# Kernel optimization log

Measured on AMD Instinct MI355X. Metric: run time of the kernel, lower is better.

Reference implementation:

```python
import jax, jax.numpy as jnp
import numpy as np

N_IN, N_H = 512, 1024

def setup_inputs() -> dict:
    key = jax.random.key(0)
    ks = jax.random.split(key, 20)
    s_in = 1.0 / np.sqrt(N_IN)
    s_h = 1.0 / np.sqrt(N_H)
    inp = {
        'x': jax.random.normal(ks[0], (64, 256, N_IN), jnp.float32),
        'c': jax.random.normal(ks[1], (64, 256, N_H), jnp.float32),
        'h': jax.random.normal(ks[2], (64, 256, N_H), jnp.float32),
    }
    names_in = ['ii', 'if_', 'ig', 'io']
    names_h = ['hi', 'hf', 'hg', 'ho']
    k = 3
    for n in names_in:
        inp['W_' + n] = jax.random.uniform(ks[k], (N_H, N_IN), jnp.float32, -s_in, s_in); k += 1
        inp['b_' + n] = jax.random.uniform(ks[k], (N_H,), jnp.float32, -s_in, s_in); k += 1
    for n in names_h:
        inp['W_' + n] = jax.random.uniform(ks[k], (N_H, N_H), jnp.float32, -s_h, s_h); k += 1
        inp['b_' + n] = jax.random.uniform(ks[k], (N_H,), jnp.float32, -s_h, s_h); k += 1
    return inp

def reference(x, c, h,
              W_ii, b_ii, W_if_, b_if_, W_ig, b_ig, W_io, b_io,
              W_hi, b_hi, W_hf, b_hf, W_hg, b_hg, W_ho, b_ho):
    # Fuse the 4 input-side and 4 hidden-side linears into two GEMMs.
    Wx = jnp.concatenate([W_ii, W_if_, W_ig, W_io], axis=0)   # [4H, n_in]
    Wh = jnp.concatenate([W_hi, W_hf, W_hg, W_ho], axis=0)   # [4H, n_h]
    bx = jnp.concatenate([b_ii, b_if_, b_ig, b_io], axis=0)
    bh = jnp.concatenate([b_hi, b_hf, b_hg, b_ho], axis=0)
    z = jnp.einsum('sad,gd->sag', x, Wx) + jnp.einsum('sad,gd->sag', h, Wh) + bx + bh  # [S,A,4H]
    zi, zf, zg, zo = jnp.split(z, 4, axis=-1)
    i_t = jax.nn.sigmoid(zi)
    f_t = jax.nn.sigmoid(zf)
    g_t = jnp.tanh(zg)
    o_t = jax.nn.sigmoid(zo)
    c_t = f_t * c + i_t * g_t
    h_t = o_t * jnp.tanh(c_t)
    return (c_t, h_t)
```

## Files before the change

kernel.cpp:

```cpp
#include <hip/hip_runtime.h>
#include <hip/hip_bf16.h>

#define M_ROWS 16384
#define N_IN   512
#define N_HID  1024
#define K_TOT  1536
#define N_TOT  4096
#define NT     48

typedef __attribute__((ext_vector_type(4))) float f32x4;
typedef __attribute__((ext_vector_type(8))) short bf16x8;
typedef __attribute__((ext_vector_type(4))) int   i32x4;

__device__ __forceinline__ ushort f2bf(float f) {
    union { float f; unsigned u; } un; un.f = f;
    unsigned u = un.u;
    u += 0x7fffu + ((u >> 16) & 1u);
    return (ushort)(u >> 16);
}

__device__ __forceinline__ bf16x8 as_bf(i32x4 v) {
    union { i32x4 i; bf16x8 b; } u; u.i = v; return u.b;
}


__global__ void build_A(const float* __restrict__ x, const float* __restrict__ h,
                        ushort* __restrict__ A) {
    const int total = M_ROWS * K_TOT / 4;
    for (int p = blockIdx.x * blockDim.x + threadIdx.x; p < total;
         p += gridDim.x * blockDim.x) {
        int flat = p * 4;
        int row = flat / K_TOT;
        int col = flat - row * K_TOT;
        const float* src = (col < N_IN)
            ? (x + (size_t)row * N_IN + col)
            : (h + (size_t)row * N_HID + (col - N_IN));
        float4 v = *(const float4*)src;
        ushort4 o;
        o.x = f2bf(v.x); o.y = f2bf(v.y); o.z = f2bf(v.z); o.w = f2bf(v.w);
        *(ushort4*)(A + flat) = o;
    }
}

__global__ void build_W(const float* __restrict__ Wii, const float* __restrict__ Wif,
                        const float* __restrict__ Wig, const float* __restrict__ Wio,
                        const float* __restrict__ Whi, const float* __restrict__ Whf,
                        const float* __restrict__ Whg, const float* __restrict__ Who,
                        ushort* __restrict__ Wp) {
    const int total = N_TOT * K_TOT / 4;
    for (int p = blockIdx.x * blockDim.x + threadIdx.x; p < total;
         p += gridDim.x * blockDim.x) {
        int flat = p * 4;
        int prow = flat / K_TOT;
        int col = flat - prow * K_TOT;
        int bn  = prow >> 8;
        int r   = prow & 255;
        int wcn = r >> 6;
        int g   = (r >> 4) & 3;
        int u   = r & 15;
        int j   = bn * 64 + wcn * 16 + u;
        const float* src;
        if (col < N_IN) {
            const float* Wx = (g == 0) ? Wii : (g == 1) ? Wif : (g == 2) ? Wig : Wio;
            src = Wx + (size_t)j * N_IN + col;
        } else {
            const float* Wh = (g == 0) ? Whi : (g == 1) ? Whf : (g == 2) ? Whg : Who;
            src = Wh + (size_t)j * N_HID + (col - N_IN);
        }
        float4 v = *(const float4*)src;
        ushort4 o;
        o.x = f2bf(v.x); o.y = f2bf(v.y); o.z = f2bf(v.z); o.w = f2bf(v.w);
        *(ushort4*)(Wp + flat) = o;
    }
}

__global__ void build_bias(const float* __restrict__ bii, const float* __restrict__ bif,
                           const float* __restrict__ big, const float* __restrict__ bio,
                           const float* __restrict__ bhi, const float* __restrict__ bhf,
                           const float* __restrict__ bhg, const float* __restrict__ bho,
                           float* __restrict__ bias) {
    int n = blockIdx.x * blockDim.x + threadIdx.x;
    if (n >= N_TOT) return;
    int g = n >> 10, j = n & 1023;
    const float* bx = (g == 0) ? bii : (g == 1) ? bif : (g == 2) ? big : bio;
    const float* bh = (g == 0) ? bhi : (g == 1) ? bhf : (g == 2) ? bhg : bho;
    bias[n] = bx[j] + bh[j];
}


__device__ __forceinline__ float sigmoid_f(float z) {
    return 1.f / (1.f + __expf(-z));
}
__device__ __forceinline__ float tanh_f(float z) {
    z = fminf(fmaxf(z, -15.f), 15.f);
    float e = __expf(2.f * z);
    return (e - 1.f) / (e + 1.f);
}

__global__ __launch_bounds__(512, 1) void lstm_gemm(
        const ushort* __restrict__ A, const ushort* __restrict__ W,
        const float* __restrict__ bias, const float* __restrict__ cin,
        float* __restrict__ outc, float* __restrict__ outh) {
    __shared__ ushort sA[4][256 * 32];
    __shared__ ushort sB[4][256 * 32];

    const int tid  = threadIdx.x;
    const int wid  = tid >> 6;
    const int lane = tid & 63;
    const int wr  = wid >> 2;
    const int wcn = wid & 3;
    const int m0 = blockIdx.x * 256;
    const int n0 = blockIdx.y * 256;

    f32x4 acc[8][4] = {};

    const int srow = tid >> 2;
    const int fch  = (tid & 3) ^ ((tid >> 3) & 3);
    const ushort* gA = A + (size_t)(m0 + srow) * K_TOT + fch * 8;
    const ushort* gB = W + (size_t)(n0 + srow) * K_TOT + fch * 8;

#define GLDS(gptr, lptr) __builtin_amdgcn_global_load_lds(                     \
        (const __attribute__((address_space(1))) void*)(gptr),                 \
        (__attribute__((address_space(3))) void*)(lptr), 16, 0, 0)

#define STAGE(db, kt) do {                                                     \
    GLDS(gA + (size_t)(kt) * 32,                  &sA[db][tid * 8]);           \
    GLDS(gA + (size_t)128 * K_TOT + (size_t)(kt) * 32, &sA[db][4096 + tid * 8]); \
    GLDS(gB + (size_t)(kt) * 32,                  &sB[db][tid * 8]);           \
    GLDS(gB + (size_t)128 * K_TOT + (size_t)(kt) * 32, &sB[db][4096 + tid * 8]); \
} while (0)

    const int lrow = lane & 15;
    const int cb0  = lane >> 4;
    const int csw2 = (lrow >> 1) & 3;
    const unsigned aByte = (unsigned)(((wr * 128 + lrow) * 32 + ((cb0 ^ csw2) * 8)) * 2);
    const unsigned bByte = (unsigned)(((wcn * 64  + lrow) * 32 + ((cb0 ^ csw2) * 8)) * 2);

#define DSR(dst, addr, IMM) asm volatile(                                      \
    "ds_read_b128 %0, %1 offset:" IMM : "=&v"(dst) : "v"(addr))

#define READS(afX, bfX, db) do {                                               \
    unsigned aAd = (unsigned)(uintptr_t)                                       \
        (__attribute__((address_space(3))) ushort*)&sA[db][0] + aByte;         \
    unsigned bAd = (unsigned)(uintptr_t)                                       \
        (__attribute__((address_space(3))) ushort*)&sB[db][0] + bByte;         \
    i32x4 r0, r1, r2, r3, r4, r5, r6, r7, s0, s1, s2, s3;                      \
    DSR(r0, aAd, "0");    DSR(r1, aAd, "1024");                                \
    DSR(r2, aAd, "2048"); DSR(r3, aAd, "3072");                                \
    DSR(r4, aAd, "4096"); DSR(r5, aAd, "5120");                                \
    DSR(r6, aAd, "6144"); DSR(r7, aAd, "7168");                                \
    DSR(s0, bAd, "0");    DSR(s1, bAd, "1024");                                \
    DSR(s2, bAd, "2048"); DSR(s3, bAd, "3072");                                \
    afX[0] = as_bf(r0); afX[1] = as_bf(r1); afX[2] = as_bf(r2);                \
    afX[3] = as_bf(r3); afX[4] = as_bf(r4); afX[5] = as_bf(r5);                \
    afX[6] = as_bf(r6); afX[7] = as_bf(r7);                                    \
    bfX[0] = as_bf(s0); bfX[1] = as_bf(s1); bfX[2] = as_bf(s2);                \
    bfX[3] = as_bf(s3);                                                        \
} while (0)

#define WAIT12() do {                                                          \
    asm volatile("s_waitcnt lgkmcnt(12)");                                     \
    __builtin_amdgcn_sched_barrier(0);                                         \
} while (0)

#define WAIT0() do {                                                           \
    asm volatile("s_waitcnt lgkmcnt(0)");                                      \
    __builtin_amdgcn_sched_barrier(0);                                         \
} while (0)

#define MFMAS(afX, bfX) do {                                                   \
    __builtin_amdgcn_s_setprio(1);                                             \
    _Pragma("unroll")                                                          \
    for (int m = 0; m < 8; ++m)                                                \
        _Pragma("unroll")                                                      \
        for (int n = 0; n < 4; ++n)                                            \
            acc[m][n] = __builtin_amdgcn_mfma_f32_16x16x32_bf16(               \
                afX[m], bfX[n], acc[m][n], 0, 0, 0);                           \
    __builtin_amdgcn_s_setprio(0);                                             \
} while (0)

#define BARX() __builtin_amdgcn_s_barrier()
#define VMC(n) asm volatile("s_waitcnt vmcnt(" #n ")" ::: "memory")

    bf16x8 af0[8], bfv0[4], af1[8], bfv1[4];

    STAGE(0, 0); STAGE(1, 1); STAGE(2, 2);
    VMC(4);
    BARX();
    READS(af0, bfv0, 0);

#define TILE(u, t, Fna, Fnb, Fca, Fcb) do {                                    \
    STAGE(((u) + 3) & 3, (t) + 3);                                             \
    READS(Fna, Fnb, ((u) + 1) & 3);                                            \
    WAIT12();                                                                  \
    MFMAS(Fca, Fcb);                                                           \
    VMC(4);                                                                    \
    BARX();                                                                    \
} while (0)

    for (int hh = 0; hh < 11; ++hh) {
        const int t = hh * 4;
        TILE(0, t + 0, af1, bfv1, af0, bfv0);
        TILE(1, t + 1, af0, bfv0, af1, bfv1);
        TILE(2, t + 2, af1, bfv1, af0, bfv0);
        TILE(3, t + 3, af0, bfv0, af1, bfv1);
    }
    TILE(0, 44, af1, bfv1, af0, bfv0);
    READS(af0, bfv0, 2);
    WAIT12();
    MFMAS(af1, bfv1);
    VMC(0);
    BARX();
    READS(af1, bfv1, 3);
    WAIT12();
    MFMAS(af0, bfv0);
    BARX();
    WAIT0();
    MFMAS(af1, bfv1);

    const int unit = blockIdx.y * 64 + wcn * 16 + lrow;
    const float b0 = bias[unit];
    const float b1 = bias[1024 + unit];
    const float b2 = bias[2048 + unit];
    const float b3 = bias[3072 + unit];
    const int r0 = m0 + wr * 128 + (lane >> 4) * 4;
#pragma unroll
    for (int mi = 0; mi < 8; ++mi) {
#pragma unroll
        for (int q = 0; q < 4; ++q) {
            const int row = r0 + mi * 16 + q;
            const size_t off = (size_t)row * N_HID + unit;
            float zi = acc[mi][0][q] + b0;
            float zf = acc[mi][1][q] + b1;
            float zg = acc[mi][2][q] + b2;
            float zo = acc[mi][3][q] + b3;
            float it_ = sigmoid_f(zi);
            float ft = sigmoid_f(zf);
            float gt = tanh_f(zg);
            float ot = sigmoid_f(zo);
            float ct = ft * cin[off] + it_ * gt;
            float ht = ot * tanh_f(ct);
            outc[off] = ct;
            outh[off] = ht;
        }
    }
#undef GLDS
#undef STAGE
#undef DSR
#undef READS
#undef WAIT12
#undef WAIT0
#undef MFMAS
#undef BARX
#undef VMC
#undef TILE
}


extern "C" void kernel_launch(void* const* d_in, const int* in_sizes, int n_in,
                              void* d_out, int out_size, void* d_ws, size_t ws_size,
                              hipStream_t stream) {
    const float* x = (const float*)d_in[0];
    const float* c = (const float*)d_in[1];
    const float* h = (const float*)d_in[2];
    const float* Wii = (const float*)d_in[3];  const float* bii = (const float*)d_in[4];
    const float* Wif = (const float*)d_in[5];  const float* bif = (const float*)d_in[6];
    const float* Wig = (const float*)d_in[7];  const float* big = (const float*)d_in[8];
    const float* Wio = (const float*)d_in[9];  const float* bio = (const float*)d_in[10];
    const float* Whi = (const float*)d_in[11]; const float* bhi = (const float*)d_in[12];
    const float* Whf = (const float*)d_in[13]; const float* bhf = (const float*)d_in[14];
    const float* Whg = (const float*)d_in[15]; const float* bhg = (const float*)d_in[16];
    const float* Who = (const float*)d_in[17]; const float* bho = (const float*)d_in[18];

    char* ws = (char*)d_ws;
    ushort* A_cat  = (ushort*)ws;
    ushort* W_perm = (ushort*)(ws + (size_t)M_ROWS * K_TOT * 2);
    float*  biasc  = (float*)(ws + (size_t)M_ROWS * K_TOT * 2
                                 + (size_t)N_TOT * K_TOT * 2);

    float* outc = (float*)d_out;
    float* outh = (float*)d_out + (size_t)M_ROWS * N_HID;

    hipLaunchKernelGGL(build_A, dim3(2048), dim3(256), 0, stream, x, h, A_cat);
    hipLaunchKernelGGL(build_W, dim3(1024), dim3(256), 0, stream,
                       Wii, Wif, Wig, Wio, Whi, Whf, Whg, Who, W_perm);
    hipLaunchKernelGGL(build_bias, dim3(16), dim3(256), 0, stream,
                       bii, bif, big, bio, bhi, bhf, bhg, bho, biasc);
    hipLaunchKernelGGL(lstm_gemm, dim3(M_ROWS / 256, N_TOT / 256), dim3(512), 0, stream,
                       A_cat, W_perm, biasc, c, outc, outh);
}
```

Measured before the change: 278.5 us.

## Load B fragments directly from global into registers, drop B LDS staging

B (weight) tiles are no longer staged through LDS. Each wave now loads its B MFMA fragments straight from global memory into registers, two k-steps ahead, while A keeps its 4-deep LDS ring. The aim is to halve LDS footprint and LDS read traffic, and launch bounds change to allow 2 blocks per CU. The trade-off is uncoalesced per-lane 16-byte global loads of W, duplicated across the two row-waves. The tighter register budget and reworked vmcnt accounting could also cause stalls or spills.

Result: slower. 331.7 us (+19.1%).

```diff
diff --git a/kernel.cpp b/kernel.cpp
--- a/kernel.cpp
+++ b/kernel.cpp
@@ -97,12 +97,11 @@
     return (e - 1.f) / (e + 1.f);
 }
 
-__global__ __launch_bounds__(512, 1) void lstm_gemm(
+__global__ __launch_bounds__(512, 2) void lstm_gemm(
         const ushort* __restrict__ A, const ushort* __restrict__ W,
         const float* __restrict__ bias, const float* __restrict__ cin,
         float* __restrict__ outc, float* __restrict__ outh) {
     __shared__ ushort sA[4][256 * 32];
-    __shared__ ushort sB[4][256 * 32];
 
     const int tid  = threadIdx.x;
     const int wid  = tid >> 6;
@@ -117,54 +116,55 @@
     const int srow = tid >> 2;
     const int fch  = (tid & 3) ^ ((tid >> 3) & 3);
     const ushort* gA = A + (size_t)(m0 + srow) * K_TOT + fch * 8;
-    const ushort* gB = W + (size_t)(n0 + srow) * K_TOT + fch * 8;
 
 #define GLDS(gptr, lptr) __builtin_amdgcn_global_load_lds(                     \
         (const __attribute__((address_space(1))) void*)(gptr),                 \
         (__attribute__((address_space(3))) void*)(lptr), 16, 0, 0)
 
 #define STAGE(db, kt) do {                                                     \
-    GLDS(gA + (size_t)(kt) * 32,                  &sA[db][tid * 8]);           \
+    GLDS(gA + (size_t)(kt) * 32,                       &sA[db][tid * 8]);      \
     GLDS(gA + (size_t)128 * K_TOT + (size_t)(kt) * 32, &sA[db][4096 + tid * 8]); \
-    GLDS(gB + (size_t)(kt) * 32,                  &sB[db][tid * 8]);           \
-    GLDS(gB + (size_t)128 * K_TOT + (size_t)(kt) * 32, &sB[db][4096 + tid * 8]); \
 } while (0)
 
     const int lrow = lane & 15;
     const int cb0  = lane >> 4;
     const int csw2 = (lrow >> 1) & 3;
     const unsigned aByte = (unsigned)(((wr * 128 + lrow) * 32 + ((cb0 ^ csw2) * 8)) * 2);
-    const unsigned bByte = (unsigned)(((wcn * 64  + lrow) * 32 + ((cb0 ^ csw2) * 8)) * 2);
+
+    const uintptr_t wBase = (uintptr_t)(W + (size_t)(n0 + wcn * 64 + lrow) * K_TOT + cb0 * 8);
 
 #define DSR(dst, addr, IMM) asm volatile(                                      \
     "ds_read_b128 %0, %1 offset:" IMM : "=&v"(dst) : "v"(addr))
 
-#define READS(afX, bfX, db) do {                                               \
+#define READS(afX, db) do {                                                    \
     unsigned aAd = (unsigned)(uintptr_t)                                       \
         (__attribute__((address_space(3))) ushort*)&sA[db][0] + aByte;         \
-    unsigned bAd = (unsigned)(uintptr_t)                                       \
-        (__attribute__((address_space(3))) ushort*)&sB[db][0] + bByte;         \
-    i32x4 r0, r1, r2, r3, r4, r5, r6, r7, s0, s1, s2, s3;                      \
+    i32x4 r0, r1, r2, r3, r4, r5, r6, r7;                                      \
     DSR(r0, aAd, "0");    DSR(r1, aAd, "1024");                                \
     DSR(r2, aAd, "2048"); DSR(r3, aAd, "3072");                                \
     DSR(r4, aAd, "4096"); DSR(r5, aAd, "5120");                                \
     DSR(r6, aAd, "6144"); DSR(r7, aAd, "7168");                                \
-    DSR(s0, bAd, "0");    DSR(s1, bAd, "1024");                                \
-    DSR(s2, bAd, "2048"); DSR(s3, bAd, "3072");                                \
     afX[0] = as_bf(r0); afX[1] = as_bf(r1); afX[2] = as_bf(r2);                \
     afX[3] = as_bf(r3); afX[4] = as_bf(r4); afX[5] = as_bf(r5);                \
     afX[6] = as_bf(r6); afX[7] = as_bf(r7);                                    \
-    bfX[0] = as_bf(s0); bfX[1] = as_bf(s1); bfX[2] = as_bf(s2);                \
-    bfX[3] = as_bf(s3);                                                        \
-} while (0)
-
-#define WAIT12() do {                                                          \
-    asm volatile("s_waitcnt lgkmcnt(12)");                                     \
-    __builtin_amdgcn_sched_barrier(0);                                         \
-} while (0)
-
-#define WAIT0() do {                                                           \
-    asm volatile("s_waitcnt lgkmcnt(0)");                                      \
+} while (0)
+
+#define BLOAD(bfX, kt) do {                                                    \
+    i32x4 b0_, b1_, b2_, b3_;                                                  \
+    uint64_t a0_ = (uint64_t)(wBase + (size_t)(kt) * 64);                      \
+    uint64_t a1_ = a0_ + 49152u;                                               \
+    uint64_t a2_ = a0_ + 98304u;                                               \
+    uint64_t a3_ = a0_ + 147456u;                                              \
+    asm volatile("global_load_dwordx4 %0, %1, off" : "=v"(b0_) : "v"(a0_));    \
+    asm volatile("global_load_dwordx4 %0, %1, off" : "=v"(b1_) : "v"(a1_));    \
+    asm volatile("global_load_dwordx4 %0, %1, off" : "=v"(b2_) : "v"(a2_));    \
+    asm volatile("global_load_dwordx4 %0, %1, off" : "=v"(b3_) : "v"(a3_));    \
+    bfX[0] = as_bf(b0_); bfX[1] = as_bf(b1_);                                  \
+    bfX[2] = as_bf(b2_); bfX[3] = as_bf(b3_);                                  \
+} while (0)
+
+#define WAITK(n) do {                                                          \
+    asm volatile("s_waitcnt lgkmcnt(" #n ")");                                 \
     __builtin_amdgcn_sched_barrier(0);                                         \
 } while (0)
 
@@ -182,41 +182,46 @@
 #define BARX() __builtin_amdgcn_s_barrier()
 #define VMC(n) asm volatile("s_waitcnt vmcnt(" #n ")" ::: "memory")
 
-    bf16x8 af0[8], bfv0[4], af1[8], bfv1[4];
+    bf16x8 af0[8], af1[8], bfr0[4], bfr1[4];
 
     STAGE(0, 0); STAGE(1, 1); STAGE(2, 2);
+    BLOAD(bfr0, 0); BLOAD(bfr1, 1);
+    VMC(4);
+    __builtin_amdgcn_sched_barrier(0);
+    BARX();
+    READS(af0, 0);
+
+#define TILE(u, t, Fna, Fca, Bc) do {                                          \
+    STAGE(((u) + 3) & 3, (t) + 3);                                             \
+    READS(Fna, ((u) + 1) & 3);                                                 \
+    WAITK(8);                                                                  \
+    MFMAS(Fca, Bc);                                                            \
+    BLOAD(Bc, (t) + 2);                                                        \
+    VMC(6);                                                                    \
+    BARX();                                                                    \
+} while (0)
+
+    for (int hh = 0; hh < 11; ++hh) {
+        const int t = hh * 4;
+        TILE(0, t + 0, af1, af0, bfr0);
+        TILE(1, t + 1, af0, af1, bfr1);
+        TILE(2, t + 2, af1, af0, bfr0);
+        TILE(3, t + 3, af0, af1, bfr1);
+    }
+    TILE(0, 44, af1, af0, bfr0);
+    READS(af0, 2);
+    WAITK(8);
+    MFMAS(af1, bfr1);
+    BLOAD(bfr1, 47);
     VMC(4);
     BARX();
-    READS(af0, bfv0, 0);
-
-#define TILE(u, t, Fna, Fnb, Fca, Fcb) do {                                    \
-    STAGE(((u) + 3) & 3, (t) + 3);                                             \
-    READS(Fna, Fnb, ((u) + 1) & 3);                                            \
-    WAIT12();                                                                  \
-    MFMAS(Fca, Fcb);                                                           \
-    VMC(4);                                                                    \
-    BARX();                                                                    \
-} while (0)
-
-    for (int hh = 0; hh < 11; ++hh) {
-        const int t = hh * 4;
-        TILE(0, t + 0, af1, bfv1, af0, bfv0);
-        TILE(1, t + 1, af0, bfv0, af1, bfv1);
-        TILE(2, t + 2, af1, bfv1, af0, bfv0);
-        TILE(3, t + 3, af0, bfv0, af1, bfv1);
-    }
-    TILE(0, 44, af1, bfv1, af0, bfv0);
-    READS(af0, bfv0, 2);
-    WAIT12();
-    MFMAS(af1, bfv1);
+    READS(af1, 3);
+    WAITK(8);
+    MFMAS(af0, bfr0);
     VMC(0);
     BARX();
-    READS(af1, bfv1, 3);
-    WAIT12();
-    MFMAS(af0, bfv0);
-    BARX();
-    WAIT0();
-    MFMAS(af1, bfv1);
+    WAITK(0);
+    MFMAS(af1, bfr1);
 
     const int unit = blockIdx.y * 64 + wcn * 16 + lrow;
     const float b0 = bias[unit];
@@ -248,8 +253,8 @@
 #undef STAGE
 #undef DSR
 #undef READS
-#undef WAIT12
-#undef WAIT0
+#undef BLOAD
+#undef WAITK
 #undef MFMAS
 #undef BARX
 #undef VMC
```

## Merge prep kernels into one launch and remap GEMM blocks per XCD

Applied to the files above, without the earlier changes.

Combines the three preprocessing kernels (activation concat/cast, weight permute/cast, bias sum) into a single grid-stride kernel, removing two launches. The GEMM is relaunched with a 1D grid whose block index is remapped so each XCD (block id mod 8) handles a contiguous group of M tiles across all N tiles. This is meant to improve L2 reuse of A rows within each XCD's cache. The merged prep kernel adds branching per element, and the remap assumes round-robin dispatch of blocks to XCDs.

New measurement: 270.5 us. -2.9%, faster.

```diff
diff --git a/kernel.cpp b/kernel.cpp
--- a/kernel.cpp
+++ b/kernel.cpp
@@ -24,67 +24,64 @@
 }
 
 
-__global__ void build_A(const float* __restrict__ x, const float* __restrict__ h,
-                        ushort* __restrict__ A) {
-    const int total = M_ROWS * K_TOT / 4;
-    for (int p = blockIdx.x * blockDim.x + threadIdx.x; p < total;
-         p += gridDim.x * blockDim.x) {
-        int flat = p * 4;
-        int row = flat / K_TOT;
-        int col = flat - row * K_TOT;
-        const float* src = (col < N_IN)
-            ? (x + (size_t)row * N_IN + col)
-            : (h + (size_t)row * N_HID + (col - N_IN));
-        float4 v = *(const float4*)src;
-        ushort4 o;
-        o.x = f2bf(v.x); o.y = f2bf(v.y); o.z = f2bf(v.z); o.w = f2bf(v.w);
-        *(ushort4*)(A + flat) = o;
+__global__ void prep_all(const float* __restrict__ x, const float* __restrict__ h,
+                         const float* __restrict__ Wii, const float* __restrict__ Wif,
+                         const float* __restrict__ Wig, const float* __restrict__ Wio,
+                         const float* __restrict__ Whi, const float* __restrict__ Whf,
+                         const float* __restrict__ Whg, const float* __restrict__ Who,
+                         const float* __restrict__ bii, const float* __restrict__ bif,
+                         const float* __restrict__ big, const float* __restrict__ bio,
+                         const float* __restrict__ bhi, const float* __restrict__ bhf,
+                         const float* __restrict__ bhg, const float* __restrict__ bho,
+                         ushort* __restrict__ A, ushort* __restrict__ Wp,
+                         float* __restrict__ bias) {
+    const int totalA = M_ROWS * K_TOT / 4;
+    const int totalW = N_TOT * K_TOT / 4;
+    const int totalE = totalA + totalW + N_TOT;
+    const int stride = gridDim.x * blockDim.x;
+    for (int p = blockIdx.x * blockDim.x + threadIdx.x; p < totalE; p += stride) {
+        if (p < totalA) {
+            int flat = p * 4;
+            int row = flat / K_TOT;
+            int col = flat - row * K_TOT;
+            const float* src = (col < N_IN)
+                ? (x + (size_t)row * N_IN + col)
+                : (h + (size_t)row * N_HID + (col - N_IN));
+            float4 v = *(const float4*)src;
+            ushort4 o;
+            o.x = f2bf(v.x); o.y = f2bf(v.y); o.z = f2bf(v.z); o.w = f2bf(v.w);
+            *(ushort4*)(A + flat) = o;
+        } else if (p < totalA + totalW) {
+            int q = p - totalA;
+            int flat = q * 4;
+            int prow = flat / K_TOT;
+            int col = flat - prow * K_TOT;
+            int bn  = prow >> 8;
+            int r   = prow & 255;
+            int wcn = r >> 6;
+            int g   = (r >> 4) & 3;
+            int u   = r & 15;
+            int j   = bn * 64 + wcn * 16 + u;
+            const float* src;
+            if (col < N_IN) {
+                const float* Wx = (g == 0) ? Wii : (g == 1) ? Wif : (g == 2) ? Wig : Wio;
+                src = Wx + (size_t)j * N_IN + col;
+            } else {
+                const float* Wh = (g == 0) ? Whi : (g == 1) ? Whf : (g == 2) ? Whg : Who;
+                src = Wh + (size_t)j * N_HID + (col - N_IN);
+            }
+            float4 v = *(const float4*)src;
+            ushort4 o;
+            o.x = f2bf(v.x); o.y = f2bf(v.y); o.z = f2bf(v.z); o.w = f2bf(v.w);
+            *(ushort4*)(Wp + flat) = o;
+        } else {
+            int n = p - totalA - totalW;
+            int g = n >> 10, j = n & 1023;
+            const float* bx = (g == 0) ? bii : (g == 1) ? bif : (g == 2) ? big : bio;
+            const float* bh = (g == 0) ? bhi : (g == 1) ? bhf : (g == 2) ? bhg : bho;
+            bias[n] = bx[j] + bh[j];
+        }
     }
-}
-
-__global__ void build_W(const float* __restrict__ Wii, const float* __restrict__ Wif,
-                        const float* __restrict__ Wig, const float* __restrict__ Wio,
-                        const float* __restrict__ Whi, const float* __restrict__ Whf,
-                        const float* __restrict__ Whg, const float* __restrict__ Who,
-                        ushort* __restrict__ Wp) {
-    const int total = N_TOT * K_TOT / 4;
-    for (int p = blockIdx.x * blockDim.x + threadIdx.x; p < total;
-         p += gridDim.x * blockDim.x) {
-        int flat = p * 4;
-        int prow = flat / K_TOT;
-        int col = flat - prow * K_TOT;
-        int bn  = prow >> 8;
-        int r   = prow & 255;
-        int wcn = r >> 6;
-        int g   = (r >> 4) & 3;
-        int u   = r & 15;
-        int j   = bn * 64 + wcn * 16 + u;
-        const float* src;
-        if (col < N_IN) {
-            const float* Wx = (g == 0) ? Wii : (g == 1) ? Wif : (g == 2) ? Wig : Wio;
-            src = Wx + (size_t)j * N_IN + col;
-        } else {
-            const float* Wh = (g == 0) ? Whi : (g == 1) ? Whf : (g == 2) ? Whg : Who;
-            src = Wh + (size_t)j * N_HID + (col - N_IN);
-        }
-        float4 v = *(const float4*)src;
-        ushort4 o;
-        o.x = f2bf(v.x); o.y = f2bf(v.y); o.z = f2bf(v.z); o.w = f2bf(v.w);
-        *(ushort4*)(Wp + flat) = o;
-    }
-}
-
-__global__ void build_bias(const float* __restrict__ bii, const float* __restrict__ bif,
-                           const float* __restrict__ big, const float* __restrict__ bio,
-                           const float* __restrict__ bhi, const float* __restrict__ bhf,
-                           const float* __restrict__ bhg, const float* __restrict__ bho,
-                           float* __restrict__ bias) {
-    int n = blockIdx.x * blockDim.x + threadIdx.x;
-    if (n >= N_TOT) return;
-    int g = n >> 10, j = n & 1023;
-    const float* bx = (g == 0) ? bii : (g == 1) ? bif : (g == 2) ? big : bio;
-    const float* bh = (g == 0) ? bhi : (g == 1) ? bhf : (g == 2) ? bhg : bho;
-    bias[n] = bx[j] + bh[j];
 }
 
 
@@ -109,8 +106,14 @@
     const int lane = tid & 63;
     const int wr  = wid >> 2;
     const int wcn = wid & 3;
-    const int m0 = blockIdx.x * 256;
-    const int n0 = blockIdx.y * 256;
+
+    const int lid = blockIdx.x;
+    const int xcd = lid & 7;
+    const int j_  = lid >> 3;
+    const int bx  = xcd * 8 + (j_ >> 4);
+    const int by  = j_ & 15;
+    const int m0 = bx * 256;
+    const int n0 = by * 256;
 
     f32x4 acc[8][4] = {};
 
@@ -158,13 +161,8 @@
     bfX[3] = as_bf(s3);                                                        \
 } while (0)
 
-#define WAIT12() do {                                                          \
-    asm volatile("s_waitcnt lgkmcnt(12)");                                     \
-    __builtin_amdgcn_sched_barrier(0);                                         \
-} while (0)
-
-#define WAIT0() do {                                                           \
-    asm volatile("s_waitcnt lgkmcnt(0)");                                      \
+#define WAITK(n) do {                                                          \
+    asm volatile("s_waitcnt lgkmcnt(" #n ")");                                 \
     __builtin_amdgcn_sched_barrier(0);                                         \
 } while (0)
 
@@ -192,7 +190,7 @@
 #define TILE(u, t, Fna, Fnb, Fca, Fcb) do {                                    \
     STAGE(((u) + 3) & 3, (t) + 3);                                             \
     READS(Fna, Fnb, ((u) + 1) & 3);                                            \
-    WAIT12();                                                                  \
+    WAITK(12);                                                                 \
     MFMAS(Fca, Fcb);                                                           \
     VMC(4);                                                                    \
     BARX();                                                                    \
@@ -207,18 +205,18 @@
     }
     TILE(0, 44, af1, bfv1, af0, bfv0);
     READS(af0, bfv0, 2);
-    WAIT12();
+    WAITK(12);
     MFMAS(af1, bfv1);
     VMC(0);
     BARX();
     READS(af1, bfv1, 3);
-    WAIT12();
+    WAITK(12);
     MFMAS(af0, bfv0);
     BARX();
-    WAIT0();
+    WAITK(0);
     MFMAS(af1, bfv1);
 
-    const int unit = blockIdx.y * 64 + wcn * 16 + lrow;
+    const int unit = by * 64 + wcn * 16 + lrow;
     const float b0 = bias[unit];
     const float b1 = bias[1024 + unit];
     const float b2 = bias[2048 + unit];
@@ -248,8 +246,7 @@
 #undef STAGE
 #undef DSR
 #undef READS
-#undef WAIT12
-#undef WAIT0
+#undef WAITK
 #undef MFMAS
 #undef BARX
 #undef VMC
@@ -281,11 +278,11 @@
     float* outc = (float*)d_out;
     float* outh = (float*)d_out + (size_t)M_ROWS * N_HID;
 
-    hipLaunchKernelGGL(build_A, dim3(2048), dim3(256), 0, stream, x, h, A_cat);
-    hipLaunchKernelGGL(build_W, dim3(1024), dim3(256), 0, stream,
-                       Wii, Wif, Wig, Wio, Whi, Whf, Whg, Who, W_perm);
-    hipLaunchKernelGGL(build_bias, dim3(16), dim3(256), 0, stream,
-                       bii, bif, big, bio, bhi, bhf, bhg, bho, biasc);
-    hipLaunchKernelGGL(lstm_gemm, dim3(M_ROWS / 256, N_TOT / 256), dim3(512), 0, stream,
+    hipLaunchKernelGGL(prep_all, dim3(2048), dim3(256), 0, stream,
+                       x, h,
+                       Wii, Wif, Wig, Wio, Whi, Whf, Whg, Who,
+                       bii, bif, big, bio, bhi, bhf, bhg, bho,
+                       A_cat, W_perm, biasc);
+    hipLaunchKernelGGL(lstm_gemm, dim3(1024), dim3(512), 0, stream,
                        A_cat, W_perm, biasc, c, outc, outh);
 }
```
